# Kernel tuning notes

Measured on AMD Instinct MI355X. Metric: run time of the kernel, lower is better.

## Reference

```python
import jax, jax.numpy as jnp
import numpy as np

HEADS = 16
LN_EPS = 1e-5


def _layernorm(x, w, b):
    mu = jnp.mean(x, axis=-1, keepdims=True)
    var = jnp.mean(jnp.square(x - mu), axis=-1, keepdims=True)
    return (x - mu) * jax.lax.rsqrt(var + LN_EPS) * w + b


def setup_inputs() -> dict:
    key = jax.random.key(0)
    ks = jax.random.split(key, 14)
    B, L, E, HID = 4, 4096, 1024, 4096
    s = 0.02
    return {
        "x": jax.random.normal(ks[0], (B, L, E), dtype=jnp.float32),
        "w_q": jax.random.normal(ks[1], (E, E), dtype=jnp.float32) * s,
        "w_k": jax.random.normal(ks[2], (E, E), dtype=jnp.float32) * s,
        "w_v": jax.random.normal(ks[3], (E, E), dtype=jnp.float32) * s,
        "w_o": jax.random.normal(ks[4], (E, E), dtype=jnp.float32) * s,
        "b_o": jnp.zeros((E,), dtype=jnp.float32),
        "ln1_w": jnp.ones((E,), dtype=jnp.float32),
        "ln1_b": jnp.zeros((E,), dtype=jnp.float32),
        "ln2_w": jnp.ones((E,), dtype=jnp.float32),
        "ln2_b": jnp.zeros((E,), dtype=jnp.float32),
        "w_ff1": jax.random.normal(ks[5], (E, HID), dtype=jnp.float32) * s,
        "b_ff1": jnp.zeros((HID,), dtype=jnp.float32),
        "w_ff2": jax.random.normal(ks[6], (HID, E), dtype=jnp.float32) * s,
        "b_ff2": jnp.zeros((E,), dtype=jnp.float32),
    }


def reference(x, w_q, w_k, w_v, w_o, b_o, ln1_w, ln1_b, ln2_w, ln2_b,
              w_ff1, b_ff1, w_ff2, b_ff2):
    N, L, E = x.shape
    H = HEADS
    D = E // H
    # projections -> (N, H, L, D) exactly as the torch view+permute
    q = (x @ w_q).reshape(N, L, H, D).transpose(0, 2, 1, 3)
    k = (x @ w_k).reshape(N, L, H, D).transpose(0, 2, 1, 3)
    v = (x @ w_v).reshape(N, L, H, D).transpose(0, 2, 1, 3)
    # Faithful to source: einsum subscripts applied to the PERMUTED tensors,
    # so 'q'/'k' bind to the heads axis and 'h','d' contract over (length, head_dim).
    # energy: (N, H, H)
    energy = jnp.einsum('nqhd,nkhd->nqk', q, k)
    attention = jax.nn.softmax(energy / (float(E) ** 0.5), axis=2)
    # 'k' and 'v' are independent sum indices -> out[n,q,h,d] = (sum_k att) * (sum_v v)
    out = jnp.einsum('nqk,nvhd->nqhd', attention, v)  # (N, H, L, D)
    out = out.reshape(N, L, H * D)  # row-major flatten, same as torch .reshape
    attn_out = out @ w_o + b_o
    # residual + LayerNorm (dropout is identity in eval)
    h1 = _layernorm(attn_out + x, ln1_w, ln1_b)
    ff = jax.nn.relu(h1 @ w_ff1 + b_ff1) @ w_ff2 + b_ff2
    return _layernorm(ff + h1, ln2_w, ln2_b)
```

## Files before the change

kernel.cpp:

```cpp
#include <hip/hip_runtime.h>
#include <stdint.h>
#include <stddef.h>

typedef __bf16 bf16_t;
typedef __bf16 bf16x8 __attribute__((ext_vector_type(8)));
typedef __bf16 bf16x4 __attribute__((ext_vector_type(4)));
typedef float f32x4 __attribute__((ext_vector_type(4)));

#define E_DIM 1024
#define HID_DIM 4096
#define NROWS 16384

__device__ __forceinline__ void async16(const bf16_t* g, void* l) {
    __builtin_amdgcn_global_load_lds(
        (const __attribute__((address_space(1))) void*)g,
        (__attribute__((address_space(3))) void*)l,
        16, 0, 0);
}

__global__ void detect_dtype(const unsigned int* __restrict__ ln1_w_raw, int* __restrict__ flag) {
    if (threadIdx.x == 0) {
        *flag = (ln1_w_raw[0] == 0x3F800000u) ? 0 : 1;
    }
}

__device__ __forceinline__ float load_in(const void* p, size_t idx, int isb) {
    if (isb) return (float)((const bf16_t*)p)[idx];
    return ((const float*)p)[idx];
}

struct VecArgs {
    const void* p[7];
    float* o[7];
    int n[7];
};

__global__ __launch_bounds__(256) void convert_vecs(VecArgs a, const int* __restrict__ dflag) {
    int isb = *dflag;
    int seg = blockIdx.y;
    int i = blockIdx.x * 256 + threadIdx.x;
    if (i < a.n[seg]) a.o[seg][i] = load_in(a.p[seg], (size_t)i, isb);
}

__global__ __launch_bounds__(256) void convert_x(const void* __restrict__ in, bf16_t* __restrict__ out,
                                                 const int* __restrict__ dflag) {
    int isb = *dflag;
    size_t i = ((size_t)blockIdx.x * 256 + threadIdx.x) * 8;
    if (isb) {
        *(bf16x8*)(out + i) = *((const bf16x8*)((const bf16_t*)in + i));
    } else {
        const float* f = (const float*)in + i;
        bf16x8 v;
#pragma unroll
        for (int j = 0; j < 8; j++) v[j] = (bf16_t)f[j];
        *(bf16x8*)(out + i) = v;
    }
}

__global__ void transpose_to_bf16(const void* __restrict__ in, bf16_t* __restrict__ out,
                                  int R, int C, const int* __restrict__ dflag) {
    int isb = *dflag;
    __shared__ bf16_t tile[32][33];
    int c0 = blockIdx.x * 32, r0 = blockIdx.y * 32;
    int tx = threadIdx.x, ty = threadIdx.y;
#pragma unroll
    for (int i = 0; i < 32; i += 8)
        tile[ty + i][tx] = (bf16_t)load_in(in, (size_t)(r0 + ty + i) * C + (c0 + tx), isb);
    __syncthreads();
#pragma unroll
    for (int i = 0; i < 32; i += 8)
        out[(size_t)(c0 + ty + i) * R + (r0 + tx)] = tile[tx][ty + i];
}

__global__ void fold_wv(const void* __restrict__ w_v, bf16_t* __restrict__ w_vs_t,
                        const int* __restrict__ dflag) {
    int isb = *dflag;
    int d = threadIdx.x;
    int e = blockIdx.x;
    float s = 0.f;
#pragma unroll
    for (int i = 0; i < 16; i++)
        s += load_in(w_v, (size_t)e * 1024 + i * 64 + d, isb);
    w_vs_t[((size_t)d << 10) + e] = (bf16_t)s;
}

template <int BM, int BN, int SWZ_G, bool RELU, bool OUT_BF16, bool HAS_BIAS>
__global__ __launch_bounds__(256) void gemm_bt(const bf16_t* __restrict__ A,
                                               const bf16_t* __restrict__ Bt,
                                               const float* __restrict__ bias,
                                               void* __restrict__ Cv,
                                               int M, int N, int K) {
    constexpr int BK = 64;
    constexpr int WM = BM / 2;
    constexpr int WN = BN / 2;
    constexpr int TM = WM / 16;
    constexpr int TN = WN / 16;
    __shared__ __align__(16) bf16_t As[BM][BK];
    __shared__ __align__(16) bf16_t Bs[BN][BK];

    const int tid = threadIdx.x;
    const int lane = tid & 63;
    const int wid = tid >> 6;
    const int wr = wid >> 1, wc = wid & 1;
    const int lm = lane & 15, quad = lane >> 4;
    const int lm7 = lm & 7;

    int bx = blockIdx.x, by = blockIdx.y;
    if (SWZ_G > 0) {
        const int flat = by * gridDim.x + bx;
        const int S = SWZ_G * gridDim.x;
        const int g = flat / S, r = flat % S;
        bx = r / SWZ_G;
        by = g * SWZ_G + (r % SWZ_G);
    }
    const int bm = by * BM, bn = bx * BN;

    const int rsub = lane >> 3;
    const int csub = ((lane & 7) ^ rsub) << 3;

    f32x4 acc[TM][TN];
#pragma unroll
    for (int i = 0; i < TM; i++)
#pragma unroll
        for (int j = 0; j < TN; j++) acc[i][j] = (f32x4){0.f, 0.f, 0.f, 0.f};

    const bf16_t* Ap = A + (size_t)bm * K + csub;
    const bf16_t* Bp = Bt + (size_t)bn * K + csub;

    for (int k0 = 0; k0 < K; k0 += BK) {
#pragma unroll
        for (int cc = 0; cc < BM / 32; cc++) {
            const int c = cc * 4 + wid;
            async16(Ap + (size_t)(c * 8 + rsub) * K + k0, (char*)&As[0][0] + c * 1024);
        }
#pragma unroll
        for (int cc = 0; cc < BN / 32; cc++) {
            const int c = cc * 4 + wid;
            async16(Bp + (size_t)(c * 8 + rsub) * K + k0, (char*)&Bs[0][0] + c * 1024);
        }
        __syncthreads();

#pragma unroll
        for (int kk = 0; kk < 2; kk++) {
            bf16x8 af[TM], bfr[TN];
#pragma unroll
            for (int i = 0; i < TM; i++) {
                const int row = wr * WM + i * 16 + lm;
                const int pb = ((kk * 4 + quad) ^ lm7) << 3;
                af[i] = *(const bf16x8*)(&As[row][pb]);
            }
#pragma unroll
            for (int j = 0; j < TN; j++) {
                const int row = wc * WN + j * 16 + lm;
                const int pb = ((kk * 4 + quad) ^ lm7) << 3;
                bfr[j] = *(const bf16x8*)(&Bs[row][pb]);
            }
#pragma unroll
            for (int i = 0; i < TM; i++)
#pragma unroll
                for (int j = 0; j < TN; j++)
                    acc[i][j] = __builtin_amdgcn_mfma_f32_16x16x32_bf16(af[i], bfr[j], acc[i][j], 0, 0, 0);
        }
        __syncthreads();
    }

    const int gm0 = bm + wr * WM, gn0 = bn + wc * WN;
#pragma unroll
    for (int i = 0; i < TM; i++) {
#pragma unroll
        for (int j = 0; j < TN; j++) {
            const int col = gn0 + j * 16 + lm;
            float bv = HAS_BIAS ? bias[col] : 0.f;
#pragma unroll
            for (int r = 0; r < 4; r++) {
                const int row = gm0 + i * 16 + quad * 4 + r;
                float v = acc[i][j][r] + bv;
                if (RELU) v = fmaxf(v, 0.f);
                if (OUT_BF16)
                    ((bf16_t*)Cv)[(size_t)row * N + col] = (bf16_t)v;
                else
                    ((float*)Cv)[(size_t)row * N + col] = v;
            }
        }
    }
}

__device__ __forceinline__ void block_reduce2(float& s, float& s2, float* red, int tid) {
#pragma unroll
    for (int o = 32; o > 0; o >>= 1) {
        s += __shfl_down(s, o, 64);
        s2 += __shfl_down(s2, o, 64);
    }
    const int wid = tid >> 6;
    if ((tid & 63) == 0) { red[wid] = s; red[4 + wid] = s2; }
    __syncthreads();
    s = red[0] + red[1] + red[2] + red[3];
    s2 = red[4] + red[5] + red[6] + red[7];
}

__global__ __launch_bounds__(256) void ln1_fused(const float* __restrict__ attn,
                                                 const bf16_t* __restrict__ xbf,
                                                 const float* __restrict__ w,
                                                 const float* __restrict__ b,
                                                 bf16_t* __restrict__ h1) {
    const int row = blockIdx.x;
    const int n = row >> 12;
    const int lp = row & 4095;
    const float* arow = attn + (((size_t)(n << 8) + (lp & 255)) << 10);
    const bf16_t* xrow = xbf + ((size_t)row << 10);
    const int tid = threadIdx.x;
    const int c4 = tid << 2;
    __shared__ float red[8];
    f32x4 a = *(const f32x4*)(arow + c4);
    bf16x4 xv = *(const bf16x4*)(xrow + c4);
    float v[4];
    float s = 0.f, s2 = 0.f;
#pragma unroll
    for (int u = 0; u < 4; u++) {
        float val = a[u] + (float)xv[u];
        v[u] = val; s += val; s2 += val * val;
    }
    block_reduce2(s, s2, red, tid);
    const float mu = s * (1.f / 1024.f);
    const float var = s2 * (1.f / 1024.f) - mu * mu;
    const float rstd = rsqrtf(var + 1e-5f);
    f32x4 wv = *(const f32x4*)(w + c4);
    f32x4 bv = *(const f32x4*)(b + c4);
    bf16x4 hv;
#pragma unroll
    for (int u = 0; u < 4; u++)
        hv[u] = (bf16_t)((v[u] - mu) * rstd * wv[u] + bv[u]);
    *(bf16x4*)(h1 + ((size_t)row << 10) + c4) = hv;
}

__global__ __launch_bounds__(256) void ln2_fused(const bf16_t* __restrict__ ff,
                                                 const bf16_t* __restrict__ h1,
                                                 const float* __restrict__ w,
                                                 const float* __restrict__ b,
                                                 void* __restrict__ outp,
                                                 const int* __restrict__ dflag,
                                                 int row0) {
    const int isb = *dflag;
    const int row = blockIdx.x;
    const int tid = threadIdx.x;
    const int c4 = tid << 2;
    __shared__ float red[8];
    bf16x4 fv = *(const bf16x4*)(ff + ((size_t)row << 10) + c4);
    bf16x4 hv = *(const bf16x4*)(h1 + ((size_t)row << 10) + c4);
    float v[4];
    float s = 0.f, s2 = 0.f;
#pragma unroll
    for (int u = 0; u < 4; u++) {
        float val = (float)fv[u] + (float)hv[u];
        v[u] = val; s += val; s2 += val * val;
    }
    block_reduce2(s, s2, red, tid);
    const float mu = s * (1.f / 1024.f);
    const float var = s2 * (1.f / 1024.f) - mu * mu;
    const float rstd = rsqrtf(var + 1e-5f);
    f32x4 wv = *(const f32x4*)(w + c4);
    f32x4 bv = *(const f32x4*)(b + c4);
    const size_t base = ((size_t)(row0 + row) << 10) + c4;
    if (isb) {
        bf16x4 ov;
#pragma unroll
        for (int u = 0; u < 4; u++) ov[u] = (bf16_t)((v[u] - mu) * rstd * wv[u] + bv[u]);
        *(bf16x4*)((bf16_t*)outp + base) = ov;
    } else {
        f32x4 ov;
#pragma unroll
        for (int u = 0; u < 4; u++) ov[u] = (v[u] - mu) * rstd * wv[u] + bv[u];
        *(f32x4*)((float*)outp + base) = ov;
    }
}

extern "C" void kernel_launch(void* const* d_in, const int* in_sizes, int n_in,
                              void* d_out, int out_size, void* d_ws, size_t ws_size,
                              hipStream_t stream) {
    char* ws = (char*)d_ws;
    const size_t MB = 1u << 20;

    int*    dflag   = (int*)ws;
    float*  vec0    = (float*)(ws + 4096);
    float*  vec_b_o   = vec0 + 0 * 4096;
    float*  vec_bff1  = vec0 + 1 * 4096;
    float*  vec_bff2  = vec0 + 2 * 4096;
    float*  vec_ln1w  = vec0 + 3 * 4096;
    float*  vec_ln1b  = vec0 + 4 * 4096;
    float*  vec_ln2w  = vec0 + 5 * 4096;
    float*  vec_ln2b  = vec0 + 6 * 4096;
    bf16_t* w_vs_t  = (bf16_t*)(ws + 256 * 1024);
    bf16_t* w_o_t   = (bf16_t*)(ws + 1 * MB);
    bf16_t* w_ff1_t = (bf16_t*)(ws + 3 * MB);
    bf16_t* w_ff2_t = (bf16_t*)(ws + 11 * MB);
    bf16_t* vsum    = (bf16_t*)(ws + 19 * MB);
    float*  attn    = (float*)(ws + 21 * MB);
    bf16_t* xbf     = (bf16_t*)(ws + 25 * MB);
    bf16_t* h1      = (bf16_t*)(ws + 57 * MB);
    bf16_t* hidden  = (bf16_t*)(ws + 89 * MB);

    int chunk;
    if (ws_size >= 250 * MB)      chunk = 16384;
    else if (ws_size >= 170 * MB) chunk = 8192;
    else                          chunk = 4096;
    bf16_t* ffbuf = (bf16_t*)(ws + 89 * MB + (size_t)chunk * HID_DIM * sizeof(bf16_t));

    detect_dtype<<<1, 64, 0, stream>>>((const unsigned int*)d_in[6], dflag);

    VecArgs va;
    va.p[0] = d_in[5];  va.o[0] = vec_b_o;  va.n[0] = 1024;
    va.p[1] = d_in[11]; va.o[1] = vec_bff1; va.n[1] = 4096;
    va.p[2] = d_in[13]; va.o[2] = vec_bff2; va.n[2] = 1024;
    va.p[3] = d_in[6];  va.o[3] = vec_ln1w; va.n[3] = 1024;
    va.p[4] = d_in[7];  va.o[4] = vec_ln1b; va.n[4] = 1024;
    va.p[5] = d_in[8];  va.o[5] = vec_ln2w; va.n[5] = 1024;
    va.p[6] = d_in[9];  va.o[6] = vec_ln2b; va.n[6] = 1024;
    convert_vecs<<<dim3(16, 7), 256, 0, stream>>>(va, dflag);

    convert_x<<<8192, 256, 0, stream>>>(d_in[0], xbf, dflag);

    transpose_to_bf16<<<dim3(32, 32),  dim3(32, 8), 0, stream>>>(d_in[4],  w_o_t,   1024, 1024, dflag);
    transpose_to_bf16<<<dim3(128, 32), dim3(32, 8), 0, stream>>>(d_in[10], w_ff1_t, 1024, 4096, dflag);
    transpose_to_bf16<<<dim3(32, 128), dim3(32, 8), 0, stream>>>(d_in[12], w_ff2_t, 4096, 1024, dflag);
    fold_wv<<<1024, 64, 0, stream>>>(d_in[3], w_vs_t, dflag);

    gemm_bt<128, 64, 0, false, true, false><<<dim3(1, 128), 256, 0, stream>>>(
        xbf, w_vs_t, nullptr, vsum, NROWS, 64, E_DIM);

    gemm_bt<128, 128, 0, false, false, true><<<dim3(8, 8), 256, 0, stream>>>(
        vsum, w_o_t, vec_b_o, attn, 1024, 1024, 1024);

    ln1_fused<<<NROWS, 256, 0, stream>>>(attn, xbf, vec_ln1w, vec_ln1b, h1);

    for (int r0 = 0; r0 < NROWS; r0 += chunk) {
        const bf16_t* h1c = h1 + (size_t)r0 * E_DIM;
        gemm_bt<128, 128, 32, true, true, true><<<dim3(HID_DIM / 128, chunk / 128), 256, 0, stream>>>(
            h1c, w_ff1_t, vec_bff1, hidden, chunk, HID_DIM, E_DIM);
        gemm_bt<128, 128, 32, false, true, true><<<dim3(E_DIM / 128, chunk / 128), 256, 0, stream>>>(
            hidden, w_ff2_t, vec_bff2, ffbuf, chunk, E_DIM, HID_DIM);
        ln2_fused<<<chunk, 256, 0, stream>>>(ffbuf, h1c, vec_ln2w, vec_ln2b, d_out, dflag, r0);
    }
}
```

Baseline: 571.8 us.

## Add 256x256-tile 8-wave GEMM with ping-pong staging for FFN matmuls

Adds a new gemm256 kernel that computes 256x256 output tiles with 512 threads (8 waves, each owning 128x64). It double-buffers LDS, interleaves async global-to-LDS loads with MFMA phases, and uses setprio and barriers to schedule loads against compute. The two FFN GEMMs switch from the 128x128 kernel to this one. The goal is more data reuse per tile and better overlap of loads with math. In exchange it uses 128KB of LDS and many registers per block, and launches fewer blocks per chunk.

```diff
diff --git a/kernel.cpp b/kernel.cpp
--- a/kernel.cpp
+++ b/kernel.cpp
@@ -169,6 +169,190 @@
     for (int i = 0; i < TM; i++) {
 #pragma unroll
         for (int j = 0; j < TN; j++) {
+            const int col = gn0 + j * 16 + lm;
+            float bv = HAS_BIAS ? bias[col] : 0.f;
+#pragma unroll
+            for (int r = 0; r < 4; r++) {
+                const int row = gm0 + i * 16 + quad * 4 + r;
+                float v = acc[i][j][r] + bv;
+                if (RELU) v = fmaxf(v, 0.f);
+                if (OUT_BF16)
+                    ((bf16_t*)Cv)[(size_t)row * N + col] = (bf16_t)v;
+                else
+                    ((float*)Cv)[(size_t)row * N + col] = v;
+            }
+        }
+    }
+}
+
+template <int SWZ_G, bool RELU, bool OUT_BF16, bool HAS_BIAS>
+__global__ __launch_bounds__(512, 2) void gemm256(const bf16_t* __restrict__ A,
+                                                  const bf16_t* __restrict__ Bt,
+                                                  const float* __restrict__ bias,
+                                                  void* __restrict__ Cv,
+                                                  int M, int N, int K) {
+    constexpr int BK = 64;
+    __shared__ __align__(16) bf16_t As[2][256][BK];
+    __shared__ __align__(16) bf16_t Bs[2][256][BK];
+
+    const int tid = threadIdx.x;
+    const int lane = tid & 63;
+    const int wid = tid >> 6;
+    const int wr = wid >> 2;
+    const int wc = wid & 3;
+    const int lm = lane & 15, quad = lane >> 4;
+    const int lm7 = lm & 7;
+    const int rsub = lane >> 3;
+    const int csub = ((lane & 7) ^ rsub) << 3;
+
+    int bx = blockIdx.x, by = blockIdx.y;
+    if (SWZ_G > 0) {
+        const int flat = by * gridDim.x + bx;
+        const int S = SWZ_G * gridDim.x;
+        const int g = flat / S, r = flat % S;
+        bx = r / SWZ_G;
+        by = g * SWZ_G + (r % SWZ_G);
+    }
+    const int bm = by * 256, bn = bx * 256;
+
+    const bf16_t* Ap = A + (size_t)bm * K + csub;
+    const bf16_t* Bp = Bt + (size_t)bn * K + csub;
+    const int c0 = wid * 2;
+
+#define STAGE_A(b, h, kt) do { \
+        const size_t ko = (size_t)(kt) * BK; \
+        async16(Ap + (size_t)((h) * 128 + c0 * 8 + rsub) * K + ko, \
+                (char*)(&As[(b)][0][0]) + (h) * 16384 + c0 * 1024); \
+        async16(Ap + (size_t)((h) * 128 + (c0 + 1) * 8 + rsub) * K + ko, \
+                (char*)(&As[(b)][0][0]) + (h) * 16384 + (c0 + 1) * 1024); \
+    } while (0)
+#define STAGE_B(b, h, kt) do { \
+        const size_t ko = (size_t)(kt) * BK; \
+        async16(Bp + (size_t)((h) * 128 + c0 * 8 + rsub) * K + ko, \
+                (char*)(&Bs[(b)][0][0]) + (h) * 16384 + c0 * 1024); \
+        async16(Bp + (size_t)((h) * 128 + (c0 + 1) * 8 + rsub) * K + ko, \
+                (char*)(&Bs[(b)][0][0]) + (h) * 16384 + (c0 + 1) * 1024); \
+    } while (0)
+
+    f32x4 acc[8][4];
+#pragma unroll
+    for (int i = 0; i < 8; i++)
+#pragma unroll
+        for (int j = 0; j < 4; j++) acc[i][j] = (f32x4){0.f, 0.f, 0.f, 0.f};
+
+    auto ldA = [&](int b, int im, int kk) -> bf16x8 {
+        const int row = wr * 128 + im * 16 + lm;
+        const int pb = ((kk * 4 + quad) ^ lm7) << 3;
+        return *(const bf16x8*)(&As[b][row][pb]);
+    };
+    auto ldB = [&](int b, int jn, int kk) -> bf16x8 {
+        const int row = wc * 64 + jn * 16 + lm;
+        const int pb = ((kk * 4 + quad) ^ lm7) << 3;
+        return *(const bf16x8*)(&Bs[b][row][pb]);
+    };
+
+    const int nt = K / BK;
+
+    STAGE_A(0, 0, 0); STAGE_A(0, 1, 0);
+    STAGE_B(0, 0, 0); STAGE_B(0, 1, 0);
+    if (nt > 1) {
+        STAGE_B(1, 0, 1); STAGE_B(1, 1, 1);
+        asm volatile("s_waitcnt vmcnt(4)" ::: "memory");
+    } else {
+        asm volatile("s_waitcnt vmcnt(0)" ::: "memory");
+    }
+    __builtin_amdgcn_s_barrier();
+
+    bf16x8 af[4][2], bfr[4][2];
+    for (int t = 0; t < nt; ++t) {
+        const int cur = t & 1, nxt = cur ^ 1;
+
+#pragma unroll
+        for (int im = 0; im < 4; ++im)
+#pragma unroll
+            for (int kk = 0; kk < 2; ++kk) af[im][kk] = ldA(cur, im, kk);
+#pragma unroll
+        for (int jn = 0; jn < 2; ++jn)
+#pragma unroll
+            for (int kk = 0; kk < 2; ++kk) bfr[jn][kk] = ldB(cur, jn, kk);
+        if (t + 1 < nt) STAGE_A(nxt, 0, t + 1);
+        __builtin_amdgcn_s_barrier();
+        asm volatile("s_waitcnt lgkmcnt(0)" ::: "memory");
+        __builtin_amdgcn_sched_barrier(0);
+        __builtin_amdgcn_s_setprio(1);
+#pragma unroll
+        for (int kk = 0; kk < 2; ++kk)
+#pragma unroll
+            for (int i = 0; i < 4; ++i)
+#pragma unroll
+                for (int j = 0; j < 2; ++j)
+                    acc[i][j] = __builtin_amdgcn_mfma_f32_16x16x32_bf16(af[i][kk], bfr[j][kk], acc[i][j], 0, 0, 0);
+        __builtin_amdgcn_s_setprio(0);
+        __builtin_amdgcn_s_barrier();
+
+#pragma unroll
+        for (int jn = 2; jn < 4; ++jn)
+#pragma unroll
+            for (int kk = 0; kk < 2; ++kk) bfr[jn][kk] = ldB(cur, jn, kk);
+        if (t + 1 < nt) STAGE_A(nxt, 1, t + 1);
+        __builtin_amdgcn_s_barrier();
+        asm volatile("s_waitcnt lgkmcnt(0)" ::: "memory");
+        __builtin_amdgcn_sched_barrier(0);
+        __builtin_amdgcn_s_setprio(1);
+#pragma unroll
+        for (int kk = 0; kk < 2; ++kk)
+#pragma unroll
+            for (int i = 0; i < 4; ++i)
+#pragma unroll
+                for (int j = 2; j < 4; ++j)
+                    acc[i][j] = __builtin_amdgcn_mfma_f32_16x16x32_bf16(af[i][kk], bfr[j][kk], acc[i][j], 0, 0, 0);
+        __builtin_amdgcn_s_setprio(0);
+        __builtin_amdgcn_s_barrier();
+
+#pragma unroll
+        for (int im = 0; im < 4; ++im)
+#pragma unroll
+            for (int kk = 0; kk < 2; ++kk) af[im][kk] = ldA(cur, im + 4, kk);
+        if (t + 2 < nt) STAGE_B(cur, 0, t + 2);
+        __builtin_amdgcn_s_barrier();
+        asm volatile("s_waitcnt lgkmcnt(0)" ::: "memory");
+        __builtin_amdgcn_sched_barrier(0);
+        __builtin_amdgcn_s_setprio(1);
+#pragma unroll
+        for (int kk = 0; kk < 2; ++kk)
+#pragma unroll
+            for (int i = 0; i < 4; ++i)
+#pragma unroll
+                for (int j = 2; j < 4; ++j)
+                    acc[4 + i][j] = __builtin_amdgcn_mfma_f32_16x16x32_bf16(af[i][kk], bfr[j][kk], acc[4 + i][j], 0, 0, 0);
+        __builtin_amdgcn_s_setprio(0);
+        __builtin_amdgcn_s_barrier();
+
+        if (t + 2 < nt) STAGE_B(cur, 1, t + 2);
+        __builtin_amdgcn_s_setprio(1);
+#pragma unroll
+        for (int kk = 0; kk < 2; ++kk)
+#pragma unroll
+            for (int i = 0; i < 4; ++i)
+#pragma unroll
+                for (int j = 0; j < 2; ++j)
+                    acc[4 + i][j] = __builtin_amdgcn_mfma_f32_16x16x32_bf16(af[i][kk], bfr[j][kk], acc[4 + i][j], 0, 0, 0);
+        __builtin_amdgcn_s_setprio(0);
+        if (t + 2 < nt) {
+            asm volatile("s_waitcnt vmcnt(4)" ::: "memory");
+        } else {
+            asm volatile("s_waitcnt vmcnt(0)" ::: "memory");
+        }
+        __builtin_amdgcn_s_barrier();
+    }
+#undef STAGE_A
+#undef STAGE_B
+
+    const int gm0 = bm + wr * 128, gn0 = bn + wc * 64;
+#pragma unroll
+    for (int i = 0; i < 8; i++) {
+#pragma unroll
+        for (int j = 0; j < 4; j++) {
             const int col = gn0 + j * 16 + lm;
             float bv = HAS_BIAS ? bias[col] : 0.f;
 #pragma unroll
@@ -334,9 +518,9 @@
 
     for (int r0 = 0; r0 < NROWS; r0 += chunk) {
         const bf16_t* h1c = h1 + (size_t)r0 * E_DIM;
-        gemm_bt<128, 128, 32, true, true, true><<<dim3(HID_DIM / 128, chunk / 128), 256, 0, stream>>>(
+        gemm256<16, true, true, true><<<dim3(HID_DIM / 256, chunk / 256), 512, 0, stream>>>(
             h1c, w_ff1_t, vec_bff1, hidden, chunk, HID_DIM, E_DIM);
-        gemm_bt<128, 128, 32, false, true, true><<<dim3(E_DIM / 128, chunk / 128), 256, 0, stream>>>(
+        gemm256<16, false, true, true><<<dim3(E_DIM / 256, chunk / 256), 512, 0, stream>>>(
             hidden, w_ff2_t, vec_bff2, ffbuf, chunk, E_DIM, HID_DIM);
         ln2_fused<<<chunk, 256, 0, stream>>>(ffbuf, h1c, vec_ln2w, vec_ln2b, d_out, dflag, r0);
     }
```

Result: faster. 505.2 us (-11.7%).
